# Kernel tuning notes

Measured on AMD Instinct MI355X. Metric: run time of the kernel, lower is better.

## Reference

```python
import jax, jax.numpy as jnp
import numpy as np
import math

# ---------- real Clebsch-Gordan coupling tables (computed once, tiny) ----------
def _cg(j1, m1, j2, m2, j3, m3):
    if m1 + m2 != m3 or j3 < abs(j1 - j2) or j3 > j1 + j2:
        return 0.0
    f = math.factorial
    pre = ((2 * j3 + 1) * f(j3 + j1 - j2) * f(j3 - j1 + j2) * f(j1 + j2 - j3) / f(j1 + j2 + j3 + 1)) ** 0.5
    pre *= (f(j3 + m3) * f(j3 - m3) * f(j1 - m1) * f(j1 + m1) * f(j2 - m2) * f(j2 + m2)) ** 0.5
    s = 0.0
    for k in range(0, j1 + j2 - j3 + 1):
        d = (k, j1 + j2 - j3 - k, j1 - m1 - k, j2 + m2 - k, j3 - j2 + m1 + k, j3 - j1 - m2 + k)
        if min(d) < 0:
            continue
        den = 1
        for t in d:
            den *= f(t)
        s += (-1) ** k / den
    return pre * s

def _Q(l):  # complex->real spherical-harmonic change of basis
    Q = np.zeros((2 * l + 1, 2 * l + 1), dtype=complex)
    Q[l, l] = 1.0
    s = 2 ** -0.5
    for m in range(1, l + 1):
        Q[l + m, l + m] = (-1) ** m * s
        Q[l + m, l - m] = s
        Q[l - m, l + m] = -1j * (-1) ** m * s
        Q[l - m, l - m] = 1j * s
    return Q

def _K(l1, l2, l3):  # real coupling tensor [2l3+1, 2l1+1, 2l2+1]
    C = np.zeros((2 * l3 + 1, 2 * l1 + 1, 2 * l2 + 1), dtype=complex)
    for M3 in range(-l3, l3 + 1):
        for M1 in range(-l1, l1 + 1):
            for M2 in range(-l2, l2 + 1):
                C[M3 + l3, M1 + l1, M2 + l2] = _cg(l1, M1, l2, M2, l3, M3)
    K = np.einsum('cC,aA,bB,CAB->cab', _Q(l3).conj(), _Q(l1), _Q(l2), C)
    K = K.imag if np.abs(K.imag).max() > np.abs(K.real).max() else K.real
    return np.asarray(K, dtype=np.float32)

# the 9 'uvu' instructions (in_l, edge_l, out_l) with multiplicities (weight_numel=144)
_PATHS = [(0, 0, 0), (0, 2, 2), (1, 0, 1), (1, 2, 1), (1, 2, 2), (2, 0, 2), (2, 2, 0), (2, 2, 1), (2, 2, 2)]
_KT = [jnp.asarray(_K(*p)) for p in _PATHS]
_MULS = [32, 32, 16, 16, 16, 8, 8, 8, 8]
_SPLITS = np.cumsum(_MULS)[:-1].tolist()
NEI = 8
EPS = 1e-5

def _sh(u):  # component-normalized real SH of unit vectors, l=0..2 (m order -l..l, l=1 -> y,z,x)
    x, y, z = u[:, 0], u[:, 1], u[:, 2]
    sh0 = jnp.ones_like(x)[:, None]
    sh1 = np.float32(3 ** 0.5) * jnp.stack([y, z, x], -1)
    s15 = np.float32(15 ** 0.5)
    s5 = np.float32(5 ** 0.5)
    sh2 = jnp.stack([s15 * x * y, s15 * y * z, 0.5 * s5 * (3 * z * z - 1.0), s15 * x * z, 0.5 * s15 * (x * x - y * y)], -1)
    return sh0, sh1, sh2

def _path(xs, sh, wp, Kt):  # xs [E,u,2l1+1], sh [E,2l2+1], Kt [2l3+1,2l1+1,2l2+1] -> [E,u,2l3+1]
    return jnp.einsum('eui,ej,oij->euo', xs, sh, Kt) * wp[None, :, None]

def _layer(x0, x1, x2, pos, src, dst, w, W0, W1, W2, bw0, bb0, bw1, bw2, N):
    ev = pos[dst] - pos[src]
    u = ev / (jnp.linalg.norm(ev, axis=1, keepdims=True) + 1e-12)
    sh0, sh1, sh2 = _sh(u)
    s0 = x0[src][:, :, None]  # [E,32,1]
    s1 = x1[src]              # [E,16,3]
    s2 = x2[src]              # [E,8,5]
    ws = jnp.split(w, _SPLITS)
    p1 = _path(s0, sh0, ws[0], _KT[0])
    p2 = _path(s0, sh2, ws[1], _KT[1])
    p3 = _path(s1, sh0, ws[2], _KT[2])
    p4 = _path(s1, sh2, ws[3], _KT[3])
    p5 = _path(s1, sh2, ws[4], _KT[4])
    p6 = _path(s2, sh0, ws[5], _KT[5])
    p7 = _path(s2, sh2, ws[6], _KT[6])
    p8 = _path(s2, sh2, ws[7], _KT[7])
    p9 = _path(s2, sh2, ws[8], _KT[8])
    m0 = jnp.concatenate([p1, p7], 1)          # [E,40,1]
    m1 = jnp.concatenate([p3, p4, p8], 1)      # [E,40,3]
    m2 = jnp.concatenate([p2, p5, p6, p9], 1)  # [E,64,5]
    a0 = jax.ops.segment_sum(m0, dst, num_segments=N)
    a1 = jax.ops.segment_sum(m1, dst, num_segments=N)
    a2 = jax.ops.segment_sum(m2, dst, num_segments=N)
    y0 = (a0[:, :, 0] @ W0) * np.float32(1.0 / 40 ** 0.5)
    y1 = jnp.einsum('num,uv->nvm', a1, W1) * np.float32(1.0 / 40 ** 0.5)
    y2 = jnp.einsum('num,uv->nvm', a2, W2) * np.float32(1.0 / 64 ** 0.5)
    # equivariant batchnorm (training stats): scalars -> standard BN, l>0 -> norm BN
    f = y0 - y0.mean(0)
    y0 = f / jnp.sqrt((f * f).mean(0) + EPS) * bw0 + bb0
    y1 = y1 / jnp.sqrt((y1 * y1).mean(axis=(0, 2)) + EPS)[None, :, None] * bw1[None, :, None]
    y2 = y2 / jnp.sqrt((y2 * y2).mean(axis=(0, 2)) + EPS)[None, :, None] * bw2[None, :, None]
    return y0, y1, y2

def _forward(positions, W_emb, tp_w, lin_W0, lin_W1, lin_W2, bn_w0, bn_b0, bn_w1, bn_w2, Wf1, Wf2, bf2, Wf3, bf3):
    B, P, _ = positions.shape
    N = B * P
    pos = positions.reshape(N, 3)
    # kNN graph from dense cdist + topk (indices are not differentiated)
    pg = jax.lax.stop_gradient(pos)
    sq = jnp.sum(pg * pg, 1)
    d2 = sq[:, None] + sq[None, :] - 2.0 * (pg @ pg.T)
    _, idx = jax.lax.top_k(-d2, NEI + 1)  # smallest distances; col 0 is self
    src = jnp.repeat(jnp.arange(N), NEI)
    dst = idx[:, 1:].reshape(-1)
    x0 = jnp.ones((N, 1), jnp.float32) @ W_emb  # embedding: only 0e->0e path exists
    x1 = jnp.zeros((N, 16, 3), jnp.float32)
    x2 = jnp.zeros((N, 8, 5), jnp.float32)
    for l in range(3):
        y0, y1, y2 = _layer(x0, x1, x2, pos, src, dst, tp_w[l], lin_W0[l], lin_W1[l], lin_W2[l],
                            bn_w0[l], bn_b0[l], bn_w1[l], bn_w2[l], N)
        x0 = jax.nn.relu(y0) + x0
        x1 = jax.nn.relu(y1) + x1
        x2 = jax.nn.relu(y2) + x2
    h = jax.nn.relu((x0 @ Wf1) * np.float32(1.0 / 32 ** 0.5))  # scalar part -> 32x0e
    h = jax.nn.relu(h @ Wf2 + bf2)
    out = (h @ Wf3 + bf3).reshape(B, P, 2)
    return out

def setup_inputs() -> dict:
    key = jax.random.key(0)
    ks = jax.random.split(key, 16)
    B, P = 4, 2048
    return {
        'positions': jax.random.normal(ks[0], (B, P, 3), jnp.float32) * 3.0,
        'W_emb': jax.random.normal(ks[1], (1, 32), jnp.float32),
        'tp_w': jax.random.normal(ks[2], (3, 144), jnp.float32),
        'lin_W0': jax.random.normal(ks[3], (3, 40, 32), jnp.float32),
        'lin_W1': jax.random.normal(ks[4], (3, 40, 16), jnp.float32),
        'lin_W2': jax.random.normal(ks[5], (3, 64, 8), jnp.float32),
        'bn_w0': 1.0 + 0.05 * jax.random.normal(ks[6], (3, 32), jnp.float32),
        'bn_b0': jnp.zeros((3, 32), jnp.float32),
        'bn_w1': 1.0 + 0.05 * jax.random.normal(ks[7], (3, 16), jnp.float32),
        'bn_w2': 1.0 + 0.05 * jax.random.normal(ks[8], (3, 8), jnp.float32),
        'Wf1': jax.random.normal(ks[9], (32, 32), jnp.float32),
        'Wf2': jax.random.normal(ks[10], (32, 16), jnp.float32) * 0.2,
        'bf2': jax.random.normal(ks[11], (16,), jnp.float32) * 0.1,
        'Wf3': jax.random.normal(ks[12], (16, 2), jnp.float32) * 0.2,
        'bf3': jax.random.normal(ks[13], (2,), jnp.float32) * 0.1,
    }

def reference(positions, W_emb, tp_w, lin_W0, lin_W1, lin_W2, bn_w0, bn_b0, bn_w1, bn_w2, Wf1, Wf2, bf2, Wf3, bf3):
    return _forward(positions, W_emb, tp_w, lin_W0, lin_W1, lin_W2, bn_w0, bn_b0, bn_w1, bn_w2, Wf1, Wf2, bf2, Wf3, bf3)
```

## Files before the change

kernel.cpp:

```cpp
#include <hip/hip_runtime.h>
#include <math.h>

#define NN 8192
#define REV_CAP 48
#define KNN_CAP 384
#define PF 12

static const size_t OFF_K     = 0;
static const size_t OFF_CNT   = 512;
static const size_t OFF_REV   = 8704;
static const size_t OFF_STATS = 401920;
static const size_t OFF_XF    = 406528;
static const size_t OFF_YF    = 1389568;
static const size_t WS_FLOATS = 2372608;

__device__ double dfact(int n){ double r=1.0; for(int i=2;i<=n;++i) r*=(double)i; return r; }

__device__ double dcg(int j1,int m1,int j2,int m2,int j3,int m3){
  if (m1+m2!=m3) return 0.0;
  if (j3 < abs(j1-j2) || j3 > j1+j2) return 0.0;
  double pre = sqrt((double)(2*j3+1)*dfact(j3+j1-j2)*dfact(j3-j1+j2)*dfact(j1+j2-j3)/dfact(j1+j2+j3+1));
  pre *= sqrt(dfact(j3+m3)*dfact(j3-m3)*dfact(j1-m1)*dfact(j1+m1)*dfact(j2-m2)*dfact(j2+m2));
  double s=0.0;
  for(int k=0;k<=j1+j2-j3;++k){
    int d1=j1+j2-j3-k, d2=j1-m1-k, d3=j2+m2-k, d4=j3-j2+m1+k, d5=j3-j1-m2+k;
    if(d1<0||d2<0||d3<0||d4<0||d5<0) continue;
    double den = dfact(k)*dfact(d1)*dfact(d2)*dfact(d3)*dfact(d4)*dfact(d5);
    s += ((k&1)? -1.0: 1.0)/den;
  }
  return pre*s;
}

__device__ int qrow(int l,int r,int* col,double* re,double* im){
  const double s = 0.70710678118654752440;
  if (r==l){ col[0]=l; re[0]=1.0; im[0]=0.0; return 1; }
  if (r>l){ int m=r-l;
    col[0]=l+m; re[0]=((m&1)?-s:s); im[0]=0.0;
    col[1]=l-m; re[1]=s;            im[1]=0.0;
  } else { int m=l-r;
    col[0]=l+m; re[0]=0.0; im[0]=((m&1)? s : -s);
    col[1]=l-m; re[1]=0.0; im[1]=s;
  }
  return 2;
}

__global__ __launch_bounds__(256) void k_setup(const float* __restrict__ pos,
        const float* __restrict__ W_emb, float* __restrict__ Kbuf,
        float* __restrict__ xf,
        float* __restrict__ xs, float* __restrict__ ys, float* __restrict__ zs,
        float* __restrict__ qs,
        int* __restrict__ cnt){
  int idx = blockIdx.x*256 + threadIdx.x;
  if (idx < 983040) { const int c = idx%120; xf[idx] = (c<32)? W_emb[c] : 0.f; return; }
  idx -= 983040;
  if (idx < 8192) {
    const float x=pos[3*idx], y=pos[3*idx+1], z=pos[3*idx+2];
    xs[idx]=x; ys[idx]=y; zs[idx]=z; qs[idx]=0.5f*(x*x+y*y+z*z);
    return;
  }
  idx -= 8192;
  if (idx < 8192) { cnt[idx]=0; return; }
  idx -= 8192;
  if (idx >= 405) return;

  const int tid = idx;
  const int sizes[9]={1,25,9,45,75,25,25,75,125};
  const int l1s[9]={0,0,1,1,1,2,2,2,2};
  const int l2s[9]={0,2,0,2,2,0,2,2,2};
  const int l3s[9]={0,2,1,1,2,2,0,1,2};
  int p=0, rem=tid;
  for(p=0;p<9;++p){ if(rem < sizes[p]) break; rem -= sizes[p]; }
  const int l1=l1s[p], l2=l2s[p], l3=l3s[p];
  const int n1=2*l1+1, n2=2*l2+1;
  const int c = rem/(n1*n2); const int r2 = rem%(n1*n2); const int a=r2/n2; const int b=r2%n2;

  int c3[2],c1[2],c2[2]; double re3[2],im3[2],re1[2],im1[2],re2[2],im2[2];
  const int nc3 = qrow(l3,c,c3,re3,im3);
  const int nc1 = qrow(l1,a,c1,re1,im1);
  const int nc2 = qrow(l2,b,c2,re2,im2);

  double accRe=0, accIm=0;
  for(int i3=0;i3<nc3;++i3){
    const double q3re=re3[i3], q3im=-im3[i3];
    for(int i1=0;i1<nc1;++i1){
      const double pre_re = q3re*re1[i1] - q3im*im1[i1];
      const double pre_im = q3re*im1[i1] + q3im*re1[i1];
      for(int i2=0;i2<nc2;++i2){
        const double cgv = dcg(l1, c1[i1]-l1, l2, c2[i2]-l2, l3, c3[i3]-l3);
        if (cgv==0.0) continue;
        accRe += (pre_re*re2[i2] - pre_im*im2[i2])*cgv;
        accIm += (pre_re*im2[i2] + pre_im*re2[i2])*cgv;
      }
    }
  }
  const bool useImag = ((l1+l2+l3)&1)!=0;
  Kbuf[tid] = (float)(useImag? accIm : accRe);
}

__global__ __launch_bounds__(256) void k_knn8(const float* __restrict__ xs,
                                              const float* __restrict__ ys,
                                              const float* __restrict__ zs,
                                              const float* __restrict__ qs,
                                              int* __restrict__ cnt, int* __restrict__ rev){
  const int lane = threadIdx.x & 63;
  const int w    = threadIdx.x >> 6;
  const int node = blockIdx.x*4 + w;
  __shared__ float sdist[4][KNN_CAP];
  __shared__ int   sidx[4][KNN_CAP];
  __shared__ int   scount[4];
  if (threadIdx.x < 4) scount[threadIdx.x]=0;
  __syncthreads();

  const float px = xs[node], py = ys[node], pz = zs[node];

  float m1 = INFINITY, m2 = INFINITY;
  for(int c=0;c<4;++c){
    const int base = (c*64 + lane)*4;
    const float4 fx = *(const float4*)(xs + base);
    const float4 fy = *(const float4*)(ys + base);
    const float4 fz = *(const float4*)(zs + base);
    const float4 fq = *(const float4*)(qs + base);
    float ss[4];
    ss[0] = fmaf(-px,fx.x, fmaf(-py,fy.x, fmaf(-pz,fz.x, fq.x)));
    ss[1] = fmaf(-px,fx.y, fmaf(-py,fy.y, fmaf(-pz,fz.y, fq.y)));
    ss[2] = fmaf(-px,fx.z, fmaf(-py,fy.z, fmaf(-pz,fz.z, fq.z)));
    ss[3] = fmaf(-px,fx.w, fmaf(-py,fy.w, fmaf(-pz,fz.w, fq.w)));
    #pragma unroll
    for(int q=0;q<4;++q){
      const float hi = fmaxf(m1, ss[q]);
      m1 = fminf(m1, ss[q]);
      m2 = fminf(m2, hi);
    }
  }
  float T = INFINITY;
  for(int r=0;r<9;++r){
    float v = m1; int l = lane;
    #pragma unroll
    for(int s=32;s>0;s>>=1){
      const float ov=__shfl_xor(v,s,64); const int ol=__shfl_xor(l,s,64);
      if (ov<v || (ov==v && ol<l)){ v=ov; l=ol; }
    }
    T = v;
    if (lane==l){ m1=m2; m2=INFINITY; }
  }

  for(int c=0;c<32;++c){
    const int base = (c*64 + lane)*4;
    const float4 fx = *(const float4*)(xs + base);
    const float4 fy = *(const float4*)(ys + base);
    const float4 fz = *(const float4*)(zs + base);
    const float4 fq = *(const float4*)(qs + base);
    float ss[4];
    ss[0] = fmaf(-px,fx.x, fmaf(-py,fy.x, fmaf(-pz,fz.x, fq.x)));
    ss[1] = fmaf(-px,fx.y, fmaf(-py,fy.y, fmaf(-pz,fz.y, fq.y)));
    ss[2] = fmaf(-px,fx.z, fmaf(-py,fy.z, fmaf(-pz,fz.z, fq.z)));
    ss[3] = fmaf(-px,fx.w, fmaf(-py,fy.w, fmaf(-pz,fz.w, fq.w)));
    #pragma unroll
    for(int q=0;q<4;++q){
      if (ss[q] <= T){
        int pos = atomicAdd(&scount[w],1);
        if (pos < KNN_CAP){ sdist[w][pos]=ss[q]; sidx[w][pos]=base+q; }
      }
    }
  }
  __syncthreads();

  int m = scount[w]; if (m > KNN_CAP) m = KNN_CAP;
  float dl[KNN_CAP/64]; int il[KNN_CAP/64];
  #pragma unroll
  for(int k=0;k<KNN_CAP/64;++k){
    const int j = lane + 64*k;
    if (j < m){ dl[k]=sdist[w][j]; il[k]=sidx[w][j]; }
    else      { dl[k]=INFINITY;    il[k]=0x7fffffff; }
  }
  for(int r=0;r<9;++r){
    float bv=dl[0]; int bi=il[0];
    #pragma unroll
    for(int k=1;k<KNN_CAP/64;++k){
      if (dl[k]<bv || (dl[k]==bv && il[k]<bi)){ bv=dl[k]; bi=il[k]; }
    }
    float v=bv; int ix=bi;
    #pragma unroll
    for(int s=32;s>0;s>>=1){
      float ov=__shfl_xor(v,s,64); int oi=__shfl_xor(ix,s,64);
      if (ov<v || (ov==v && oi<ix)){ v=ov; ix=oi; }
    }
    if (ix != node && lane==0){
      int cpos = atomicAdd(&cnt[ix],1);
      if (cpos < REV_CAP) rev[ix*REV_CAP + cpos] = node;
    }
    #pragma unroll
    for(int k=0;k<KNN_CAP/64;++k){
      if (il[k]==ix){ dl[k]=INFINITY; il[k]=0x7fffffff; }
    }
  }
}

__global__ __launch_bounds__(256) void k_msg(
  const float* __restrict__ pos,
  const int* __restrict__ cnt, const int* __restrict__ rev,
  const float* __restrict__ Kbuf,
  const float* __restrict__ xf,
  const float* __restrict__ tpw,
  const float* __restrict__ W0, const float* __restrict__ W1, const float* __restrict__ W2,
  float* __restrict__ yf)
{
  const int t = threadIdx.x;
  const int w = t >> 6;
  const int lane = t & 63;
  const int n = blockIdx.x*4 + w;

  __shared__ float KL[405];
  __shared__ float TW[144];
  __shared__ float momP[4][120];
  __shared__ float momS[4][600];
  __shared__ float aS[4][480];
  __shared__ int   eIdx[4][REV_CAP];
  __shared__ float eSh[4][5][REV_CAP];
  for(int q=t;q<405;q+=256) KL[q]=Kbuf[q];
  for(int q=t;q<144;q+=256) TW[q]=tpw[q];

  const int deg0 = cnt[n];
  const int deg = (deg0<REV_CAP)? deg0 : REV_CAP;
  const float pnx=pos[3*n], pny=pos[3*n+1], pnz=pos[3*n+2];
  const float s15 = 3.8729833462f, s5c = 2.2360679775f;
  if (lane < deg){
    const int i = rev[n*REV_CAP+lane];
    eIdx[w][lane] = i;
    const float ex = pnx - pos[3*i], ey = pny - pos[3*i+1], ez = pnz - pos[3*i+2];
    const float rn = sqrtf(ex*ex+ey*ey+ez*ez) + 1e-12f;
    const float ux=ex/rn, uy=ey/rn, uz=ez/rn;
    eSh[w][0][lane]=s15*ux*uy;
    eSh[w][1][lane]=s15*uy*uz;
    eSh[w][2][lane]=0.5f*s5c*(3.f*uz*uz-1.f);
    eSh[w][3][lane]=s15*ux*uz;
    eSh[w][4][lane]=0.5f*s15*(ux*ux-uy*uy);
  }
  __syncthreads();

  const int c0 = lane*2;
  float mp0=0.f, mp1=0.f;
  float ms0[5], ms1[5];
  #pragma unroll
  for(int j=0;j<5;++j){ ms0[j]=0.f; ms1[j]=0.f; }

  int idxr[PF];
  #pragma unroll
  for(int k=0;k<PF;++k) idxr[k] = (k<deg)? eIdx[w][k] : 0;
  float2 fr[PF];
  if (lane<60){
    #pragma unroll
    for(int k=0;k<PF;++k) fr[k] = *(const float2*)(xf + (size_t)idxr[k]*120 + c0);
  }
  #pragma unroll
  for(int k=0;k<PF;++k){
    if (k<deg){
      const float sh0=eSh[w][0][k], sh1=eSh[w][1][k], sh2=eSh[w][2][k];
      const float sh3=eSh[w][3][k], sh4=eSh[w][4][k];
      if (lane<60){
        const float2 f = fr[k];
        mp0 += f.x; mp1 += f.y;
        ms0[0]+=f.x*sh0; ms0[1]+=f.x*sh1; ms0[2]+=f.x*sh2; ms0[3]+=f.x*sh3; ms0[4]+=f.x*sh4;
        ms1[0]+=f.y*sh0; ms1[1]+=f.y*sh1; ms1[2]+=f.y*sh2; ms1[3]+=f.y*sh3; ms1[4]+=f.y*sh4;
      }
    }
  }
  for(int e=PF;e<deg;++e){
    const int i = eIdx[w][e];
    const float sh0=eSh[w][0][e], sh1=eSh[w][1][e], sh2=eSh[w][2][e];
    const float sh3=eSh[w][3][e], sh4=eSh[w][4][e];
    if (lane<60){
      const float2 f = *(const float2*)(xf + (size_t)i*120 + c0);
      mp0 += f.x; mp1 += f.y;
      ms0[0]+=f.x*sh0; ms0[1]+=f.x*sh1; ms0[2]+=f.x*sh2; ms0[3]+=f.x*sh3; ms0[4]+=f.x*sh4;
      ms1[0]+=f.y*sh0; ms1[1]+=f.y*sh1; ms1[2]+=f.y*sh2; ms1[3]+=f.y*sh3; ms1[4]+=f.y*sh4;
    }
  }
  if (lane<60){
    momP[w][c0]=mp0; momP[w][c0+1]=mp1;
    #pragma unroll
    for(int j=0;j<5;++j){ momS[w][c0*5+j]=ms0[j]; momS[w][(c0+1)*5+j]=ms1[j]; }
  }
  __syncthreads();

  float acc[14];
  #pragma unroll
  for(int k=0;k<14;++k) acc[k]=0.f;

  if (lane<32){
    const int u=lane;
    const float rw0=TW[u], rw1=TW[32+u];
    acc[0] = rw0 * KL[0] * momP[w][u];
    float m0s[5];
    #pragma unroll
    for(int j=0;j<5;++j) m0s[j]=momS[w][u*5+j];
    #pragma unroll
    for(int o=0;o<5;++o){ float g=0.f;
      #pragma unroll
      for(int j=0;j<5;++j) g += KL[1+o*5+j]*m0s[j];
      acc[1+o] = rw1*g; }
  } else if (lane<48){
    const int u=lane-32;
    const float rw0=TW[64+u], rw1=TW[80+u], rw2=TW[96+u];
    float m1p[3], m1s[3][5];
    #pragma unroll
    for(int i=0;i<3;++i){
      m1p[i]=momP[w][32+u*3+i];
      #pragma unroll
      for(int j=0;j<5;++j) m1s[i][j]=momS[w][(32+u*3+i)*5+j];
    }
    #pragma unroll
    for(int o=0;o<3;++o){ float g=0.f;
      #pragma unroll
      for(int i=0;i<3;++i) g += KL[26+o*3+i]*m1p[i];
      acc[o]=rw0*g; }
    #pragma unroll
    for(int o=0;o<3;++o){ float g=0.f;
      #pragma unroll
      for(int i=0;i<3;++i)
        #pragma unroll
        for(int j=0;j<5;++j) g += KL[35+(o*3+i)*5+j]*m1s[i][j];
      acc[3+o]=rw1*g; }
    #pragma unroll
    for(int o=0;o<5;++o){ float g=0.f;
      #pragma unroll
      for(int i=0;i<3;++i)
        #pragma unroll
        for(int j=0;j<5;++j) g += KL[80+(o*3+i)*5+j]*m1s[i][j];
      acc[6+o]=rw2*g; }
  } else if (lane<56){
    const int u=lane-48;
    const float rw0=TW[112+u], rw1=TW[120+u], rw2=TW[128+u], rw3=TW[136+u];
    float m2p[5], m2s[5][5];
    #pragma unroll
    for(int i=0;i<5;++i){
      m2p[i]=momP[w][80+u*5+i];
      #pragma unroll
      for(int j=0;j<5;++j) m2s[i][j]=momS[w][(80+u*5+i)*5+j];
    }
    #pragma unroll
    for(int o=0;o<5;++o){ float g=0.f;
      #pragma unroll
      for(int i=0;i<5;++i) g += KL[155+o*5+i]*m2p[i];
      acc[o]=rw0*g; }
    { float g=0.f;
      #pragma unroll
      for(int i=0;i<5;++i)
        #pragma unroll
        for(int j=0;j<5;++j) g += KL[180+i*5+j]*m2s[i][j];
      acc[5]=rw1*g; }
    #pragma unroll
    for(int o=0;o<3;++o){ float g=0.f;
      #pragma unroll
      for(int i=0;i<5;++i)
        #pragma unroll
        for(int j=0;j<5;++j) g += KL[205+(o*5+i)*5+j]*m2s[i][j];
      acc[6+o]=rw2*g; }
    #pragma unroll
    for(int o=0;o<5;++o){ float g=0.f;
      #pragma unroll
      for(int i=0;i<5;++i)
        #pragma unroll
        for(int j=0;j<5;++j) g += KL[280+(o*5+i)*5+j]*m2s[i][j];
      acc[9+o]=rw3*g; }
  }

  if (lane<32){
    aS[w][lane] = acc[0];
    #pragma unroll
    for(int o=0;o<5;++o) aS[w][160 + lane*5+o] = acc[1+o];
  } else if (lane<48){
    const int uu=lane-32;
    #pragma unroll
    for(int m=0;m<3;++m){ aS[w][40 + uu*3+m] = acc[m]; aS[w][40 + (16+uu)*3+m] = acc[3+m]; }
    #pragma unroll
    for(int o=0;o<5;++o) aS[w][160 + (32+uu)*5+o] = acc[6+o];
  } else if (lane<56){
    const int uu=lane-48;
    aS[w][32+uu] = acc[5];
    #pragma unroll
    for(int m=0;m<3;++m) aS[w][40 + (32+uu)*3+m] = acc[6+m];
    #pragma unroll
    for(int o=0;o<5;++o){ aS[w][160 + (48+uu)*5+o] = acc[o]; aS[w][160 + (56+uu)*5+o] = acc[9+o]; }
  }
  __syncthreads();

  const float inv40 = 0.15811388300841896660f;
  for(int q=lane;q<120;q+=64){
    float out;
    if (q<32){
      float g=0.f;
      for(int uu=0;uu<40;++uu) g += aS[w][uu]*W0[uu*32+q];
      out = g*inv40;
    } else if (q<80){
      const int e=q-32, v=e/3, m=e%3;
      float g=0.f;
      for(int uu=0;uu<40;++uu) g += aS[w][40+uu*3+m]*W1[uu*16+v];
      out = g*inv40;
    } else {
      const int e=q-80, tt=e/5, m=e%5;
      float g=0.f;
      for(int uu=0;uu<64;++uu) g += aS[w][160+uu*5+m]*W2[uu*8+tt];
      out = g*0.125f;
    }
    yf[(size_t)n*120+q] = out;
  }
}

__global__ __launch_bounds__(256) void k_statp(const float* __restrict__ yf,
                                               float* __restrict__ pA, float* __restrict__ pB){
  const int ch = blockIdx.x % 96;
  const int chunk = blockIdx.x / 96;
  const int t = threadIdx.x;
  const int n0 = chunk*1024;
  __shared__ float r1[256], r2[256];
  float a1=0.f, a2=0.f;
  if (ch<32){
    for(int nn=t;nn<1024;nn+=256){ float v=yf[(size_t)(n0+nn)*120+ch]; a1+=v; a2+=v*v; }
  } else if (ch<48){
    const int v_=ch-32;
    for(int nn=t;nn<1024;nn+=256){
      #pragma unroll
      for(int m=0;m<3;++m){ float v=yf[(size_t)(n0+nn)*120+32+v_*3+m]; a2+=v*v; }
    }
  } else {
    const int t_=ch-48;
    for(int nn=t;nn<1024;nn+=256){
      #pragma unroll
      for(int m=0;m<5;++m){ float v=yf[(size_t)(n0+nn)*120+80+t_*5+m]; a2+=v*v; }
    }
  }
  r1[t]=a1; r2[t]=a2; __syncthreads();
  for(int s=128;s>0;s>>=1){ if(t<s){ r1[t]+=r1[t+s]; r2[t]+=r2[t+s]; } __syncthreads(); }
  if(t==0){ pA[ch*8+chunk]=r1[0]; pB[ch*8+chunk]=r2[0]; }
}

__global__ __launch_bounds__(256) void k_norm(const float* __restrict__ yf,
                       const float* __restrict__ pA, const float* __restrict__ pB,
                       const float* __restrict__ bw0,const float* __restrict__ bb0,
                       const float* __restrict__ bw1,const float* __restrict__ bw2,
                       float* __restrict__ xf){
  __shared__ float sc[96], sf[32];
  const int t = threadIdx.x;
  if (t<96){
    float sB=0.f;
    #pragma unroll
    for(int k=0;k<8;++k) sB += pB[t*8+k];
    float scale;
    if (t<32){
      float sA=0.f;
      #pragma unroll
      for(int k=0;k<8;++k) sA += pA[t*8+k];
      const float mean = sA*(1.f/8192.f);
      const float var  = sB*(1.f/8192.f) - mean*mean;
      const float inv  = 1.f/sqrtf(var+1e-5f);
      scale = bw0[t]*inv;
      sf[t] = bb0[t] - mean*scale;
    } else if (t<48){
      scale = bw1[t-32]/sqrtf(sB*(1.f/(8192.f*3.f))+1e-5f);
    } else {
      scale = bw2[t-48]/sqrtf(sB*(1.f/(8192.f*5.f))+1e-5f);
    }
    sc[t]=scale;
  }
  __syncthreads();
  const int idx = blockIdx.x*256 + t;
  if (idx >= NN*120) return;
  const int c = idx%120;
  const int chan = (c<32)? c : ((c<80)? 32+(c-32)/3 : 48+(c-80)/5);
  const float v = yf[idx]*sc[chan] + ((c<32)? sf[c] : 0.f);
  xf[idx] += fmaxf(v,0.f);
}

__global__ __launch_bounds__(256) void k_normmlp(const float* __restrict__ yf,
                                             const float* __restrict__ xf,
                                             const float* __restrict__ pA, const float* __restrict__ pB,
                                             const float* __restrict__ bw0,const float* __restrict__ bb0,
                                             const float* __restrict__ Wf1,const float* __restrict__ Wf2,
                                             const float* __restrict__ bf2,const float* __restrict__ Wf3,
                                             const float* __restrict__ bf3, float* __restrict__ out){
  __shared__ float w1[1024], w2[512], w3[32], b2[16], b3[2], sc0[32], sf0[32];
  const int t=threadIdx.x;
  for(int q=t;q<1024;q+=256) w1[q]=Wf1[q];
  for(int q=t;q<512;q+=256)  w2[q]=Wf2[q];
  if(t<32) w3[t]=Wf3[t];
  if(t<16) b2[t]=bf2[t];
  if(t<2)  b3[t]=bf3[t];
  if(t<32){
    float sA=0.f, sB=0.f;
    #pragma unroll
    for(int k=0;k<8;++k){ sA += pA[t*8+k]; sB += pB[t*8+k]; }
    const float mean = sA*(1.f/8192.f);
    const float var  = sB*(1.f/8192.f) - mean*mean;
    const float inv  = 1.f/sqrtf(var+1e-5f);
    sc0[t] = bw0[t]*inv;
    sf0[t] = bb0[t] - mean*sc0[t];
  }
  __syncthreads();
  const int n = blockIdx.x*256+t;
  if(n>=NN) return;
  float xv[32];
  #pragma unroll
  for(int k=0;k<32;++k){
    const float v = yf[(size_t)n*120+k]*sc0[k] + sf0[k];
    xv[k] = xf[(size_t)n*120+k] + fmaxf(v,0.f);
  }
  const float inv32 = 0.17677669529663688110f;
  float h1[32];
  #pragma unroll 4
  for(int c=0;c<32;++c){ float g=0.f;
    #pragma unroll
    for(int k=0;k<32;++k) g+=xv[k]*w1[k*32+c];
    h1[c]=fmaxf(g*inv32,0.f); }
  float h2[16];
  #pragma unroll 4
  for(int c=0;c<16;++c){ float g=b2[c];
    #pragma unroll
    for(int k=0;k<32;++k) g+=h1[k]*w2[k*16+c];
    h2[c]=fmaxf(g,0.f); }
  #pragma unroll
  for(int m=0;m<2;++m){ float g=b3[m];
    #pragma unroll
    for(int k=0;k<16;++k) g+=h2[k]*w3[k*2+m];
    out[n*2+m]=g; }
}

extern "C" void kernel_launch(void* const* d_in, const int* in_sizes, int n_in,
                              void* d_out, int out_size, void* d_ws, size_t ws_size,
                              hipStream_t stream) {
  const float* positions = (const float*)d_in[0];
  const float* W_emb  = (const float*)d_in[1];
  const float* tp_w   = (const float*)d_in[2];
  const float* lin_W0 = (const float*)d_in[3];
  const float* lin_W1 = (const float*)d_in[4];
  const float* lin_W2 = (const float*)d_in[5];
  const float* bn_w0  = (const float*)d_in[6];
  const float* bn_b0  = (const float*)d_in[7];
  const float* bn_w1  = (const float*)d_in[8];
  const float* bn_w2  = (const float*)d_in[9];
  const float* Wf1 = (const float*)d_in[10];
  const float* Wf2 = (const float*)d_in[11];
  const float* bf2 = (const float*)d_in[12];
  const float* Wf3 = (const float*)d_in[13];
  const float* bf3 = (const float*)d_in[14];

  if (ws_size < WS_FLOATS*sizeof(float)) return;

  float* ws    = (float*)d_ws;
  float* Kbuf  = ws + OFF_K;
  int*   cnt   = (int*)(ws + OFF_CNT);
  int*   rev   = (int*)(ws + OFF_REV);
  float* stats = ws + OFF_STATS;
  float* xf = ws + OFF_XF;
  float* yf = ws + OFF_YF;

  float* xs = yf;
  float* ysA = yf + NN;
  float* zs = yf + 2*NN;
  float* qs = yf + 3*NN;

  k_setup<<<3906,256,0,stream>>>(positions, W_emb, Kbuf, xf, xs, ysA, zs, qs, cnt);
  k_knn8<<<NN/4,256,0,stream>>>(xs, ysA, zs, qs, cnt, rev);

  for(int l=0;l<3;++l){
    float* pA = stats + l*1536;
    float* pB = pA + 768;
    k_msg<<<NN/4,256,0,stream>>>(positions, cnt, rev, Kbuf, xf,
                              tp_w + l*144, lin_W0 + l*40*32, lin_W1 + l*40*16, lin_W2 + l*64*8,
                              yf);
    k_statp<<<768,256,0,stream>>>(yf, pA, pB);
    if (l<2){
      k_norm<<<(NN*120+255)/256,256,0,stream>>>(yf, pA, pB,
                              bn_w0 + l*32, bn_b0 + l*32, bn_w1 + l*16, bn_w2 + l*8,
                              xf);
    }
  }
  k_normmlp<<<NN/256,256,0,stream>>>(yf, xf, stats + 2*1536, stats + 2*1536 + 768,
                              bn_w0 + 64, bn_b0 + 64,
                              Wf1, Wf2, bf2, Wf3, bf3, (float*)d_out);
}
```

Before: 298.6 us.

## Fuse batch-norm statistics reduction into message kernel via replicated atomics

Removes the separate k_statp kernel that re-read the whole yf buffer to compute per-channel sums and sums of squares. k_msg now accumulates these statistics in shared memory with atomics and flushes them into 32 replicated global slots, which spreads out atomic contention. The normalization kernels sum over the replicas, and the setup kernel zeroes the enlarged stats buffer. This saves three kernel launches and three passes over yf, at the cost of shared and global atomics and a float summation order that is no longer deterministic.

```diff
diff --git a/kernel.cpp b/kernel.cpp
--- a/kernel.cpp
+++ b/kernel.cpp
@@ -5,14 +5,15 @@
 #define REV_CAP 48
 #define KNN_CAP 384
 #define PF 12
+#define NREP 32
 
 static const size_t OFF_K     = 0;
 static const size_t OFF_CNT   = 512;
 static const size_t OFF_REV   = 8704;
 static const size_t OFF_STATS = 401920;
-static const size_t OFF_XF    = 406528;
-static const size_t OFF_YF    = 1389568;
-static const size_t WS_FLOATS = 2372608;
+static const size_t OFF_XF    = 420480;
+static const size_t OFF_YF    = 1403520;
+static const size_t WS_FLOATS = 2386560;
 
 __device__ double dfact(int n){ double r=1.0; for(int i=2;i<=n;++i) r*=(double)i; return r; }
 
@@ -49,7 +50,7 @@
         float* __restrict__ xf,
         float* __restrict__ xs, float* __restrict__ ys, float* __restrict__ zs,
         float* __restrict__ qs,
-        int* __restrict__ cnt){
+        int* __restrict__ cnt, float* __restrict__ stats){
   int idx = blockIdx.x*256 + threadIdx.x;
   if (idx < 983040) { const int c = idx%120; xf[idx] = (c<32)? W_emb[c] : 0.f; return; }
   idx -= 983040;
@@ -61,6 +62,8 @@
   idx -= 8192;
   if (idx < 8192) { cnt[idx]=0; return; }
   idx -= 8192;
+  if (idx < 18432) { stats[idx]=0.f; return; }
+  idx -= 18432;
   if (idx >= 405) return;
 
   const int tid = idx;
@@ -203,7 +206,8 @@
   const float* __restrict__ xf,
   const float* __restrict__ tpw,
   const float* __restrict__ W0, const float* __restrict__ W1, const float* __restrict__ W2,
-  float* __restrict__ yf)
+  float* __restrict__ yf,
+  float* __restrict__ statsA, float* __restrict__ statsB)
 {
   const int t = threadIdx.x;
   const int w = t >> 6;
@@ -217,8 +221,10 @@
   __shared__ float aS[4][480];
   __shared__ int   eIdx[4][REV_CAP];
   __shared__ float eSh[4][5][REV_CAP];
+  __shared__ float sA[96], sB[96];
   for(int q=t;q<405;q+=256) KL[q]=Kbuf[q];
   for(int q=t;q<144;q+=256) TW[q]=tpw[q];
+  if (t<96){ sA[t]=0.f; sB[t]=0.f; }
 
   const int deg0 = cnt[n];
   const int deg = (deg0<REV_CAP)? deg0 : REV_CAP;
@@ -388,55 +394,40 @@
   const float inv40 = 0.15811388300841896660f;
   for(int q=lane;q<120;q+=64){
     float out;
+    int chan;
     if (q<32){
       float g=0.f;
       for(int uu=0;uu<40;++uu) g += aS[w][uu]*W0[uu*32+q];
       out = g*inv40;
+      chan = q;
+      atomicAdd(&sA[q], out);
     } else if (q<80){
       const int e=q-32, v=e/3, m=e%3;
       float g=0.f;
       for(int uu=0;uu<40;++uu) g += aS[w][40+uu*3+m]*W1[uu*16+v];
       out = g*inv40;
+      chan = 32+v;
     } else {
       const int e=q-80, tt=e/5, m=e%5;
       float g=0.f;
       for(int uu=0;uu<64;++uu) g += aS[w][160+uu*5+m]*W2[uu*8+tt];
       out = g*0.125f;
-    }
+      chan = 48+tt;
+    }
+    atomicAdd(&sB[chan], out*out);
     yf[(size_t)n*120+q] = out;
   }
-}
-
-__global__ __launch_bounds__(256) void k_statp(const float* __restrict__ yf,
-                                               float* __restrict__ pA, float* __restrict__ pB){
-  const int ch = blockIdx.x % 96;
-  const int chunk = blockIdx.x / 96;
-  const int t = threadIdx.x;
-  const int n0 = chunk*1024;
-  __shared__ float r1[256], r2[256];
-  float a1=0.f, a2=0.f;
-  if (ch<32){
-    for(int nn=t;nn<1024;nn+=256){ float v=yf[(size_t)(n0+nn)*120+ch]; a1+=v; a2+=v*v; }
-  } else if (ch<48){
-    const int v_=ch-32;
-    for(int nn=t;nn<1024;nn+=256){
-      #pragma unroll
-      for(int m=0;m<3;++m){ float v=yf[(size_t)(n0+nn)*120+32+v_*3+m]; a2+=v*v; }
-    }
-  } else {
-    const int t_=ch-48;
-    for(int nn=t;nn<1024;nn+=256){
-      #pragma unroll
-      for(int m=0;m<5;++m){ float v=yf[(size_t)(n0+nn)*120+80+t_*5+m]; a2+=v*v; }
-    }
-  }
-  r1[t]=a1; r2[t]=a2; __syncthreads();
-  for(int s=128;s>0;s>>=1){ if(t<s){ r1[t]+=r1[t+s]; r2[t]+=r2[t+s]; } __syncthreads(); }
-  if(t==0){ pA[ch*8+chunk]=r1[0]; pB[ch*8+chunk]=r2[0]; }
+  __syncthreads();
+
+  if (t<96){
+    const int rep = blockIdx.x & (NREP-1);
+    if (t<32) atomicAdd(&statsA[rep*96+t], sA[t]);
+    atomicAdd(&statsB[rep*96+t], sB[t]);
+  }
 }
 
 __global__ __launch_bounds__(256) void k_norm(const float* __restrict__ yf,
-                       const float* __restrict__ pA, const float* __restrict__ pB,
+                       const float* __restrict__ statsA, const float* __restrict__ statsB,
                        const float* __restrict__ bw0,const float* __restrict__ bb0,
                        const float* __restrict__ bw1,const float* __restrict__ bw2,
                        float* __restrict__ xf){
@@ -444,13 +435,13 @@
   const int t = threadIdx.x;
   if (t<96){
     float sB=0.f;
-    #pragma unroll
-    for(int k=0;k<8;++k) sB += pB[t*8+k];
+    #pragma unroll 8
+    for(int r=0;r<NREP;++r) sB += statsB[r*96+t];
     float scale;
     if (t<32){
       float sA=0.f;
-      #pragma unroll
-      for(int k=0;k<8;++k) sA += pA[t*8+k];
+      #pragma unroll 8
+      for(int r=0;r<NREP;++r) sA += statsA[r*96+t];
       const float mean = sA*(1.f/8192.f);
       const float var  = sB*(1.f/8192.f) - mean*mean;
       const float inv  = 1.f/sqrtf(var+1e-5f);
@@ -474,7 +465,7 @@
 
 __global__ __launch_bounds__(256) void k_normmlp(const float* __restrict__ yf,
                                              const float* __restrict__ xf,
-                                             const float* __restrict__ pA, const float* __restrict__ pB,
+                                             const float* __restrict__ statsA, const float* __restrict__ statsB,
                                              const float* __restrict__ bw0,const float* __restrict__ bb0,
                                              const float* __restrict__ Wf1,const float* __restrict__ Wf2,
                                              const float* __restrict__ bf2,const float* __restrict__ Wf3,
@@ -488,8 +479,8 @@
   if(t<2)  b3[t]=bf3[t];
   if(t<32){
     float sA=0.f, sB=0.f;
-    #pragma unroll
-    for(int k=0;k<8;++k){ sA += pA[t*8+k]; sB += pB[t*8+k]; }
+    #pragma unroll 8
+    for(int r=0;r<NREP;++r){ sA += statsA[r*96+t]; sB += statsB[r*96+t]; }
     const float mean = sA*(1.f/8192.f);
     const float var  = sB*(1.f/8192.f) - mean*mean;
     const float inv  = 1.f/sqrtf(var+1e-5f);
@@ -559,23 +550,22 @@
   float* zs = yf + 2*NN;
   float* qs = yf + 3*NN;
 
-  k_setup<<<3906,256,0,stream>>>(positions, W_emb, Kbuf, xf, xs, ysA, zs, qs, cnt);
+  k_setup<<<3978,256,0,stream>>>(positions, W_emb, Kbuf, xf, xs, ysA, zs, qs, cnt, stats);
   k_knn8<<<NN/4,256,0,stream>>>(xs, ysA, zs, qs, cnt, rev);
 
   for(int l=0;l<3;++l){
-    float* pA = stats + l*1536;
-    float* pB = pA + 768;
+    float* sAb = stats + l*6144;
+    float* sBb = sAb + 3072;
     k_msg<<<NN/4,256,0,stream>>>(positions, cnt, rev, Kbuf, xf,
                               tp_w + l*144, lin_W0 + l*40*32, lin_W1 + l*40*16, lin_W2 + l*64*8,
-                              yf);
-    k_statp<<<768,256,0,stream>>>(yf, pA, pB);
+                              yf, sAb, sBb);
     if (l<2){
-      k_norm<<<(NN*120+255)/256,256,0,stream>>>(yf, pA, pB,
+      k_norm<<<(NN*120+255)/256,256,0,stream>>>(yf, sAb, sBb,
                               bn_w0 + l*32, bn_b0 + l*32, bn_w1 + l*16, bn_w2 + l*8,
                               xf);
     }
   }
-  k_normmlp<<<NN/256,256,0,stream>>>(yf, xf, stats + 2*1536, stats + 2*1536 + 768,
+  k_normmlp<<<NN/256,256,0,stream>>>(yf, xf, stats + 2*6144, stats + 2*6144 + 3072,
                               bn_w0 + 64, bn_b0 + 64,
                               Wf1, Wf2, bf2, Wf3, bf3, (float*)d_out);
 }
```

Result: no change. 304.2 us (+1.9%).
